# Performance work log

Hardware: AMD Instinct MI355X
Metric: run time of the kernel (lower is better)

## Reference

```python
import jax, jax.numpy as jnp
import numpy as np

B, TQ, TK, N = 4, 128, 512, 1024   # batch, query len, key len, key_size
QS, VS, OS = 1024, 1024, 1024      # query_size, value_size, output_size


def setup_inputs() -> dict:
    key = jax.random.key(0)
    ks = jax.random.split(key, 9)
    s_q = 1.0 / np.sqrt(QS)
    s_k = 1.0 / np.sqrt(N)
    s_o = 1.0 / np.sqrt(QS + VS)
    return {
        "query": jax.random.normal(ks[0], (B, TQ, QS), jnp.float32),
        "keys": jax.random.normal(ks[1], (B, TK, N), jnp.float32),
        "values": jax.random.normal(ks[2], (B, TK, VS), jnp.float32),
        # linear_q: query_size -> key_size
        "Wq": jax.random.normal(ks[3], (N, QS), jnp.float32) * s_q,
        "bq": jax.random.normal(ks[4], (N,), jnp.float32) * s_q,
        # linear_att: key_size -> 1
        "w_att": jax.random.normal(ks[5], (N,), jnp.float32) * s_k,
        "b_att": jax.random.normal(ks[6], (), jnp.float32) * s_k,
        # linear_out: (query_size + value_size) -> output_size
        "Wout": jax.random.normal(ks[7], (OS, QS + VS), jnp.float32) * s_o,
        "bout": jax.random.normal(ks[8], (OS,), jnp.float32) * s_o,
    }


def reference(query, keys, values, Wq, bq, w_att, b_att, Wout, bout):
    # linear_q: [b, t_q, query_size] -> [b, t_q, n]
    att_query = jnp.einsum("bqe,ne->bqn", query, Wq) + bq
    # Bahdanau additive score: tanh(q + k) then linear_att (n -> 1)
    # intermediate is [b, t_q, t_k, n] as in the original module
    sum_qk = jnp.tanh(att_query[:, :, None, :] + keys[:, None, :, :])
    scores = jnp.einsum("bqkn,n->bqk", sum_qk, w_att) + b_att  # [b, t_q, t_k]
    scores_normalized = jax.nn.softmax(scores, axis=2)
    # context = softmax(scores) @ values  (dropout is identity with p=0)
    context = jnp.einsum("bqk,bkv->bqv", scores_normalized, values)
    # linear_out on concat([query, context]) + tanh
    cat = jnp.concatenate([query, context], axis=2)  # [b, t_q, q+v]
    out = jnp.tanh(jnp.einsum("bqc,oc->bqo", cat, Wout) + bout)
    return out, scores_normalized
```

## Files before the change

### kernel.cpp

```cpp
#include <hip/hip_runtime.h>
#include <math.h>

static constexpr int B_  = 4;
static constexpr int TQ  = 128;
static constexpr int TK  = 512;
static constexpr int NN  = 1024;
static constexpr int QS  = 1024;
static constexpr int VS  = 1024;
static constexpr int OS  = 1024;

#define K2F    2.8853900817779268f
#define LOG2EF 1.4426950408889634f
#define SLICE  524288

typedef __attribute__((ext_vector_type(8))) short bf16x8;
typedef __attribute__((ext_vector_type(4))) float f32x4;

#define MFMA16(a,b,c) __builtin_amdgcn_mfma_f32_16x16x32_bf16((a),(b),(c),0,0,0)

__device__ __forceinline__ ushort bf16_rne(float x) {
    uint u = __float_as_uint(x);
    u += 0x7FFFu + ((u >> 16) & 1u);
    return (ushort)(u >> 16);
}
__device__ __forceinline__ void split2(float x, ushort& h, ushort& l) {
    ushort hh = bf16_rne(x);
    float hv = __uint_as_float((uint)hh << 16);
    h = hh;
    l = bf16_rne(x - hv);
}

__global__ __launch_bounds__(256) void cvt_all_kernel(
    const float* __restrict__ Q, const float* __restrict__ Wq,
    const float* __restrict__ Wo, const float* __restrict__ V,
    ushort* __restrict__ Qh, ushort* __restrict__ Ql,
    ushort* __restrict__ Wqh, ushort* __restrict__ Wql,
    ushort* __restrict__ Woh,
    ushort* __restrict__ Vth, ushort* __restrict__ Vtl)
{
    __shared__ float tile[64][65];
    const int bid = blockIdx.x;
    const int t = threadIdx.x;
    if (bid < 3584) {
        if (bid < 1536) {
            const float* src; ushort *h, *l; int idx;
            if (bid < 512) { src = Q;  h = Qh;  l = Ql;  idx = bid*256 + t; }
            else           { src = Wq; h = Wqh; l = Wql; idx = (bid-512)*256 + t; }
            float4 v = ((const float4*)src)[idx];
            ushort4 hh, ll;
            split2(v.x, hh.x, ll.x); split2(v.y, hh.y, ll.y);
            split2(v.z, hh.z, ll.z); split2(v.w, hh.w, ll.w);
            ((ushort4*)h)[idx] = hh;
            ((ushort4*)l)[idx] = ll;
        } else {
            int idx = (bid-1536)*256 + t;
            float4 v = ((const float4*)Wo)[idx];
            ushort4 hh;
            hh.x = bf16_rne(v.x); hh.y = bf16_rne(v.y);
            hh.z = bf16_rne(v.z); hh.w = bf16_rne(v.w);
            ((ushort4*)Woh)[idx] = hh;
        }
        return;
    }
    const int vid = bid - 3584;
    const int v0 = (vid & 15) * 64;
    const int k0 = ((vid >> 4) & 7) * 64;
    const int b  = vid >> 7;
    const float* src = V + ((size_t)b*TK + k0)*VS + v0;
    #pragma unroll
    for (int p = 0; p < 4; ++p) {
        int r = (t >> 4) + p*16, c = (t & 15) * 4;
        float4 vv = *(const float4*)(src + (size_t)r*VS + c);
        tile[r][c] = vv.x; tile[r][c+1] = vv.y; tile[r][c+2] = vv.z; tile[r][c+3] = vv.w;
    }
    __syncthreads();
    ushort* dh = Vth + (size_t)b*(VS*TK) + (size_t)v0*TK + k0;
    ushort* dl = Vtl + (size_t)b*(VS*TK) + (size_t)v0*TK + k0;
    #pragma unroll
    for (int p = 0; p < 4; ++p) {
        int vr = (t >> 4) + p*16, kc = (t & 15) * 4;
        ushort4 hh, ll;
        split2(tile[kc+0][vr], hh.x, ll.x);
        split2(tile[kc+1][vr], hh.y, ll.y);
        split2(tile[kc+2][vr], hh.z, ll.z);
        split2(tile[kc+3][vr], hh.w, ll.w);
        *(ushort4*)(dh + (size_t)vr*TK + kc) = hh;
        *(ushort4*)(dl + (size_t)vr*TK + kc) = ll;
    }
}

__global__ __launch_bounds__(256) void mfma_nt_kernel(
    const ushort* __restrict__ Ah, const ushort* __restrict__ Al,
    const ushort* __restrict__ Bh, const ushort* __restrict__ Bl,
    float* __restrict__ Cp, int lda, int ldb, int Nout, int kchunk, int bstride)
{
    __shared__ alignas(16) ushort lA[2][64][40];
    __shared__ alignas(16) ushort lB[2][64][40];
    const int t = threadIdx.x;
    const int m0 = blockIdx.y * 64, n0 = blockIdx.x * 64, kz = blockIdx.z;
    const int k0 = kz * kchunk;
    const int batch = m0 >> 7;
    const ushort* bhp = Bh + (size_t)batch * bstride;
    const ushort* blp = Bl + (size_t)batch * bstride;
    const int srow = t >> 2, skc = (t & 3) * 8;
    const int lane = t & 63, w = t >> 6;
    const int wm = (w >> 1) * 32, wn = (w & 1) * 32;
    const int fr = lane & 15, fg = (lane >> 4) * 8;

    f32x4 acc00 = {0,0,0,0}, acc01 = {0,0,0,0}, acc10 = {0,0,0,0}, acc11 = {0,0,0,0};

    for (int kb = k0; kb < k0 + kchunk; kb += 32) {
        uint4 va_h = *(const uint4*)(Ah  + (size_t)(m0+srow)*lda + kb + skc);
        uint4 va_l = *(const uint4*)(Al  + (size_t)(m0+srow)*lda + kb + skc);
        uint4 vb_h = *(const uint4*)(bhp + (size_t)(n0+srow)*ldb + kb + skc);
        uint4 vb_l = *(const uint4*)(blp + (size_t)(n0+srow)*ldb + kb + skc);
        *(uint4*)&lA[0][srow][skc] = va_h;
        *(uint4*)&lA[1][srow][skc] = va_l;
        *(uint4*)&lB[0][srow][skc] = vb_h;
        *(uint4*)&lB[1][srow][skc] = vb_l;
        __syncthreads();
        bf16x8 ah0 = *(const bf16x8*)&lA[0][wm + fr     ][fg];
        bf16x8 ah1 = *(const bf16x8*)&lA[0][wm + 16 + fr][fg];
        bf16x8 al0 = *(const bf16x8*)&lA[1][wm + fr     ][fg];
        bf16x8 al1 = *(const bf16x8*)&lA[1][wm + 16 + fr][fg];
        bf16x8 bh0 = *(const bf16x8*)&lB[0][wn + fr     ][fg];
        bf16x8 bh1 = *(const bf16x8*)&lB[0][wn + 16 + fr][fg];
        bf16x8 bl0 = *(const bf16x8*)&lB[1][wn + fr     ][fg];
        bf16x8 bl1 = *(const bf16x8*)&lB[1][wn + 16 + fr][fg];
        acc00 = MFMA16(ah0, bh0, acc00);
        acc00 = MFMA16(al0, bh0, acc00);
        acc00 = MFMA16(ah0, bl0, acc00);
        acc01 = MFMA16(ah0, bh1, acc01);
        acc01 = MFMA16(al0, bh1, acc01);
        acc01 = MFMA16(ah0, bl1, acc01);
        acc10 = MFMA16(ah1, bh0, acc10);
        acc10 = MFMA16(al1, bh0, acc10);
        acc10 = MFMA16(ah1, bl0, acc10);
        acc11 = MFMA16(ah1, bh1, acc11);
        acc11 = MFMA16(al1, bh1, acc11);
        acc11 = MFMA16(ah1, bl1, acc11);
        __syncthreads();
    }
    float* o = Cp + (size_t)kz * 512 * Nout;
    const int orow = (lane >> 4) * 4;
    #pragma unroll
    for (int r2 = 0; r2 < 4; ++r2) {
        o[(size_t)(m0+wm+orow+r2)*Nout      + n0+wn+fr]      = acc00[r2];
        o[(size_t)(m0+wm+orow+r2)*Nout      + n0+wn+16+fr]   = acc01[r2];
        o[(size_t)(m0+wm+16+orow+r2)*Nout   + n0+wn+fr]      = acc10[r2];
        o[(size_t)(m0+wm+16+orow+r2)*Nout   + n0+wn+16+fr]   = acc11[r2];
    }
}

__global__ __launch_bounds__(256) void exp_combine_kernel(
    const float* __restrict__ Ap, const float* __restrict__ bias,
    float* __restrict__ E)
{
    int i = blockIdx.x * 256 + threadIdx.x;
    float4 p0 = ((const float4*)Ap)[i];
    float4 p1 = ((const float4*)(Ap + SLICE))[i];
    float4 p2 = ((const float4*)(Ap + 2*SLICE))[i];
    float4 p3 = ((const float4*)(Ap + 3*SLICE))[i];
    float4 bb = ((const float4*)bias)[i & 255];
    float4 r;
    r.x = exp2f((p0.x+p1.x+p2.x+p3.x+bb.x) * K2F);
    r.y = exp2f((p0.y+p1.y+p2.y+p3.y+bb.y) * K2F);
    r.z = exp2f((p0.z+p1.z+p2.z+p3.z+bb.z) * K2F);
    r.w = exp2f((p0.w+p1.w+p2.w+p3.w+bb.w) * K2F);
    ((float4*)E)[i] = r;
}

__global__ __launch_bounds__(256) void score_v7_kernel(
    const float* __restrict__ Ea,
    const float* __restrict__ keys,
    const float* __restrict__ watt,
    float* __restrict__ Sp)
{
    __shared__ float ea[64][66];
    __shared__ float ek[64][36];
    __shared__ float wl[64];
    const int tid = threadIdx.x;
    const int kt = blockIdx.x;
    const int qt = blockIdx.y;
    const int nh = blockIdx.z;
    const int nbeg = nh * 64;
    const int q0 = qt * 64;
    const int b  = qt >> 1;
    const int k0 = b*TK + kt*32;

    {
        const int q = tid >> 2;
        const int nc = (tid & 3) * 16;
        const float* ep = Ea + (size_t)(q0 + q)*NN + nbeg + nc;
        #pragma unroll
        for (int j4 = 0; j4 < 4; ++j4) {
            float4 ev = *(const float4*)(ep + j4*4);
            ea[nc+j4*4+0][q] = ev.x;
            ea[nc+j4*4+1][q] = ev.y;
            ea[nc+j4*4+2][q] = ev.z;
            ea[nc+j4*4+3][q] = ev.w;
        }
    }
    {
        const int k = tid >> 3;
        const int nc = (tid & 7) * 8;
        const float* kp = keys + (size_t)(k0 + k)*NN + nbeg + nc;
        #pragma unroll
        for (int j4 = 0; j4 < 2; ++j4) {
            float4 kv = *(const float4*)(kp + j4*4);
            ek[nc+j4*4+0][k] = exp2f(kv.x * K2F);
            ek[nc+j4*4+1][k] = exp2f(kv.y * K2F);
            ek[nc+j4*4+2][k] = exp2f(kv.z * K2F);
            ek[nc+j4*4+3][k] = exp2f(kv.w * K2F);
        }
    }
    if (tid < 64) wl[tid] = watt[nbeg + tid];
    __syncthreads();

    const int tx = tid & 7;
    const int ty = tid >> 3;
    float acc[2][4] = {};
    #pragma unroll 4
    for (int g = 0; g < 16; ++g) {
        float2 e0 = *(const float2*)&ea[4*g+0][ty*2];
        float2 e1 = *(const float2*)&ea[4*g+1][ty*2];
        float2 e2 = *(const float2*)&ea[4*g+2][ty*2];
        float2 e3 = *(const float2*)&ea[4*g+3][ty*2];
        float4 f0 = *(const float4*)&ek[4*g+0][tx*4];
        float4 f1 = *(const float4*)&ek[4*g+1][tx*4];
        float4 f2 = *(const float4*)&ek[4*g+2][tx*4];
        float4 f3 = *(const float4*)&ek[4*g+3][tx*4];
        float4 w4 = *(const float4*)&wl[4*g];
        float E0[2] = {e0.x, e0.y};
        float E1[2] = {e1.x, e1.y};
        float E2[2] = {e2.x, e2.y};
        float E3[2] = {e3.x, e3.y};
        float F0[4] = {f0.x, f0.y, f0.z, f0.w};
        float F1[4] = {f1.x, f1.y, f1.z, f1.w};
        float F2[4] = {f2.x, f2.y, f2.z, f2.w};
        float F3[4] = {f3.x, f3.y, f3.z, f3.w};
        #pragma unroll
        for (int i = 0; i < 2; ++i) {
            #pragma unroll
            for (int j = 0; j < 4; ++j) {
                float A  = fmaf(E0[i], F0[j], 1.0f);
                float Bv = fmaf(E1[i], F1[j], 1.0f);
                float C  = fmaf(E2[i], F2[j], 1.0f);
                float D  = fmaf(E3[i], F3[j], 1.0f);
                float n0 = fmaf(w4.x, Bv, w4.y * A);
                float n1 = fmaf(w4.z, D,  w4.w * C);
                acc[i][j] = fmaf(n0, __builtin_amdgcn_rcpf(A * Bv), acc[i][j]);
                acc[i][j] = fmaf(n1, __builtin_amdgcn_rcpf(C * D),  acc[i][j]);
            }
        }
    }
    float* o = Sp + ((size_t)nh*512 + q0 + ty*2)*TK + kt*32 + tx*4;
    #pragma unroll
    for (int i = 0; i < 2; ++i) {
        float4 r = {-2.0f*acc[i][0], -2.0f*acc[i][1], -2.0f*acc[i][2], -2.0f*acc[i][3]};
        *(float4*)(o + (size_t)i*TK) = r;
    }
}

__global__ __launch_bounds__(256) void softmax_kernel(
    const float* __restrict__ Sp, float* __restrict__ P,
    ushort* __restrict__ Ph, ushort* __restrict__ Pl)
{
    const int lane = threadIdx.x & 63;
    const int wid  = threadIdx.x >> 6;
    const int row  = blockIdx.x * 4 + wid;
    const size_t S = (size_t)512*512;
    float v[8];
    float m = -3.4e38f;
    #pragma unroll
    for (int j = 0; j < 8; ++j) {
        int k = lane + j*64;
        float s = 0.f;
        #pragma unroll
        for (int h = 0; h < 16; ++h)
            s += Sp[h*S + (size_t)row*TK + k];
        v[j] = s;
        m = fmaxf(m, v[j]);
    }
    #pragma unroll
    for (int off = 32; off; off >>= 1) m = fmaxf(m, __shfl_xor(m, off, 64));
    float sum = 0.f;
    #pragma unroll
    for (int j = 0; j < 8; ++j) { v[j] = exp2f((v[j] - m) * LOG2EF); sum += v[j]; }
    #pragma unroll
    for (int off = 32; off; off >>= 1) sum += __shfl_xor(sum, off, 64);
    float inv = 1.0f / sum;
    #pragma unroll
    for (int j = 0; j < 8; ++j) {
        int k = lane + j*64;
        float pv = v[j] * inv;
        P[(size_t)row * TK + k] = pv;
        ushort h, l; split2(pv, h, l);
        Ph[(size_t)row * TK + k] = h;
        Pl[(size_t)row * TK + k] = l;
    }
}

__global__ __launch_bounds__(256) void combine_cvt_kernel(
    const float* __restrict__ Ep, ushort* __restrict__ Ch, ushort* __restrict__ Cl)
{
    int i = blockIdx.x * 256 + threadIdx.x;
    float4 p0 = ((const float4*)Ep)[i];
    float4 p1 = ((const float4*)(Ep + SLICE))[i];
    float4 p2 = ((const float4*)(Ep + 2*SLICE))[i];
    float4 p3 = ((const float4*)(Ep + 3*SLICE))[i];
    float4 s = {p0.x+p1.x+p2.x+p3.x, p0.y+p1.y+p2.y+p3.y,
                p0.z+p1.z+p2.z+p3.z, p0.w+p1.w+p2.w+p3.w};
    ushort4 hh, ll;
    split2(s.x, hh.x, ll.x); split2(s.y, hh.y, ll.y);
    split2(s.z, hh.z, ll.z); split2(s.w, hh.w, ll.w);
    ((ushort4*)Ch)[i] = hh;
    ((ushort4*)Cl)[i] = ll;
}

__global__ __launch_bounds__(256) void mfma_out_kernel(
    const ushort* __restrict__ Qh, const ushort* __restrict__ Ql,
    const ushort* __restrict__ Cxh, const ushort* __restrict__ Cxl,
    const ushort* __restrict__ Wh,
    float* __restrict__ Fp)
{
    __shared__ alignas(16) ushort lA[2][64][40];
    __shared__ alignas(16) ushort lB[64][40];
    const int t = threadIdx.x;
    const int m0 = blockIdx.y * 64, n0 = blockIdx.x * 64, kz = blockIdx.z;
    const ushort* ah_p = (kz < 2) ? Qh : Cxh;
    const ushort* al_p = (kz < 2) ? Ql : Cxl;
    const int akoff = (kz & 1) * 512;
    const int bkoff = kz * 512;
    const int srow = t >> 2, skc = (t & 3) * 8;
    const int lane = t & 63, w = t >> 6;
    const int wm = (w >> 1) * 32, wn = (w & 1) * 32;
    const int fr = lane & 15, fg = (lane >> 4) * 8;

    f32x4 acc00 = {0,0,0,0}, acc01 = {0,0,0,0}, acc10 = {0,0,0,0}, acc11 = {0,0,0,0};

    for (int kk = 0; kk < 512; kk += 32) {
        size_t aoff = (size_t)(m0+srow)*1024 + akoff + kk + skc;
        *(uint4*)&lA[0][srow][skc] = *(const uint4*)(ah_p + aoff);
        *(uint4*)&lA[1][srow][skc] = *(const uint4*)(al_p + aoff);
        *(uint4*)&lB[srow][skc] =
            *(const uint4*)(Wh + (size_t)(n0+srow)*2048 + bkoff + kk + skc);
        __syncthreads();
        bf16x8 ah0 = *(const bf16x8*)&lA[0][wm + fr     ][fg];
        bf16x8 ah1 = *(const bf16x8*)&lA[0][wm + 16 + fr][fg];
        bf16x8 al0 = *(const bf16x8*)&lA[1][wm + fr     ][fg];
        bf16x8 al1 = *(const bf16x8*)&lA[1][wm + 16 + fr][fg];
        bf16x8 bh0 = *(const bf16x8*)&lB[wn + fr     ][fg];
        bf16x8 bh1 = *(const bf16x8*)&lB[wn + 16 + fr][fg];
        acc00 = MFMA16(ah0, bh0, acc00);
        acc00 = MFMA16(al0, bh0, acc00);
        acc01 = MFMA16(ah0, bh1, acc01);
        acc01 = MFMA16(al0, bh1, acc01);
        acc10 = MFMA16(ah1, bh0, acc10);
        acc10 = MFMA16(al1, bh0, acc10);
        acc11 = MFMA16(ah1, bh1, acc11);
        acc11 = MFMA16(al1, bh1, acc11);
        __syncthreads();
    }
    float* o = Fp + (size_t)kz * SLICE;
    const int orow = (lane >> 4) * 4;
    #pragma unroll
    for (int r2 = 0; r2 < 4; ++r2) {
        o[(size_t)(m0+wm+orow+r2)*1024    + n0+wn+fr]    = acc00[r2];
        o[(size_t)(m0+wm+orow+r2)*1024    + n0+wn+16+fr] = acc01[r2];
        o[(size_t)(m0+wm+16+orow+r2)*1024 + n0+wn+fr]    = acc10[r2];
        o[(size_t)(m0+wm+16+orow+r2)*1024 + n0+wn+16+fr] = acc11[r2];
    }
}

__global__ __launch_bounds__(256) void tanh_combine_kernel(
    const float* __restrict__ Fp, const float* __restrict__ bias,
    float* __restrict__ out)
{
    int i = blockIdx.x * 256 + threadIdx.x;
    const size_t S = (size_t)B_*TQ*OS;
    float4 p0 = ((const float4*)Fp)[i];
    float4 p1 = ((const float4*)(Fp + S))[i];
    float4 p2 = ((const float4*)(Fp + 2*S))[i];
    float4 p3 = ((const float4*)(Fp + 3*S))[i];
    float4 bb = ((const float4*)bias)[i & 255];
    float4 r;
    r.x = tanhf(p0.x + p1.x + p2.x + p3.x + bb.x);
    r.y = tanhf(p0.y + p1.y + p2.y + p3.y + bb.y);
    r.z = tanhf(p0.z + p1.z + p2.z + p3.z + bb.z);
    r.w = tanhf(p0.w + p1.w + p2.w + p3.w + bb.w);
    ((float4*)out)[i] = r;
}

extern "C" void kernel_launch(void* const* d_in, const int* in_sizes, int n_in,
                              void* d_out, int out_size, void* d_ws, size_t ws_size,
                              hipStream_t stream)
{
    const float* query  = (const float*)d_in[0];
    const float* keys   = (const float*)d_in[1];
    const float* values = (const float*)d_in[2];
    const float* Wq     = (const float*)d_in[3];
    const float* bq     = (const float*)d_in[4];
    const float* watt   = (const float*)d_in[5];
    const float* Wout   = (const float*)d_in[7];
    const float* bout   = (const float*)d_in[8];

    float* out = (float*)d_out;
    float* P   = out + (size_t)B_*TQ*OS;

    char* base = (char*)d_ws;
    const size_t MB = 1u << 20;
    ushort* Qh  = (ushort*)(base +  0*MB);
    ushort* Ql  = (ushort*)(base +  1*MB);
    ushort* Wqh = (ushort*)(base +  2*MB);
    ushort* Wql = (ushort*)(base +  4*MB);
    ushort* Woh = (ushort*)(base +  6*MB);
    ushort* Vth = (ushort*)(base + 10*MB);
    ushort* Vtl = (ushort*)(base + 14*MB);
    float*  Ap  = (float*) (base + 18*MB);
    float*  Ea  = (float*) (base + 26*MB);
    float*  Sp  = (float*) (base + 28*MB);
    ushort* Ph  = (ushort*)(base + 44*MB);
    ushort* Pl  = (ushort*)(base + 44*MB + 512*1024);
    float*  Ep  = (float*) (base + 45*MB);
    ushort* Cxh = (ushort*)(base + 53*MB);
    ushort* Cxl = (ushort*)(base + 54*MB);
    float*  Fp  = (float*) (base + 55*MB);

    cvt_all_kernel<<<dim3(4096), dim3(256), 0, stream>>>(
        query, Wq, Wout, values, Qh, Ql, Wqh, Wql, Woh, Vth, Vtl);
    mfma_nt_kernel<<<dim3(16, 8, 4), dim3(256), 0, stream>>>(
        Qh, Ql, Wqh, Wql, Ap, 1024, 1024, 1024, 256, 0);
    exp_combine_kernel<<<dim3(512), dim3(256), 0, stream>>>(Ap, bq, Ea);
    score_v7_kernel<<<dim3(16, 8, 16), dim3(256), 0, stream>>>(Ea, keys, watt, Sp);
    softmax_kernel<<<dim3(128), dim3(256), 0, stream>>>(Sp, P, Ph, Pl);
    mfma_nt_kernel<<<dim3(16, 8, 4), dim3(256), 0, stream>>>(
        Ph, Pl, Vth, Vtl, Ep, 512, 512, 1024, 128, VS*TK);
    combine_cvt_kernel<<<dim3(512), dim3(256), 0, stream>>>(Ep, Cxh, Cxl);
    mfma_out_kernel<<<dim3(16, 8, 4), dim3(256), 0, stream>>>(
        Qh, Ql, Cxh, Cxl, Woh, Fp);
    tanh_combine_kernel<<<dim3(512), dim3(256), 0, stream>>>(Fp, bout, out);
}
```

Measured before the change: 82.99 us.

## Drop low bf16 half of values and halve score partial-sum slices

The values tensor is now converted only to a high bf16 part. The P·V GEMM uses a new kernel that does two MFMAs per tile pair (Ph·Vh, Pl·Vh) instead of three, and the Vtl buffer and its writes are removed. Separately, each score block now covers two 64-wide n chunks in sequence, so there are 8 partial slices instead of 16, which reduces Sp traffic and the number of reads the softmax must sum. This trades some accuracy in the context product and some score-kernel parallelism for less memory traffic and less MFMA work.

```diff
diff --git a/kernel.cpp b/kernel.cpp
--- a/kernel.cpp
+++ b/kernel.cpp
@@ -36,7 +36,7 @@
     ushort* __restrict__ Qh, ushort* __restrict__ Ql,
     ushort* __restrict__ Wqh, ushort* __restrict__ Wql,
     ushort* __restrict__ Woh,
-    ushort* __restrict__ Vth, ushort* __restrict__ Vtl)
+    ushort* __restrict__ Vth)
 {
     __shared__ float tile[64][65];
     const int bid = blockIdx.x;
@@ -75,17 +75,15 @@
     }
     __syncthreads();
     ushort* dh = Vth + (size_t)b*(VS*TK) + (size_t)v0*TK + k0;
-    ushort* dl = Vtl + (size_t)b*(VS*TK) + (size_t)v0*TK + k0;
     #pragma unroll
     for (int p = 0; p < 4; ++p) {
         int vr = (t >> 4) + p*16, kc = (t & 15) * 4;
-        ushort4 hh, ll;
-        split2(tile[kc+0][vr], hh.x, ll.x);
-        split2(tile[kc+1][vr], hh.y, ll.y);
-        split2(tile[kc+2][vr], hh.z, ll.z);
-        split2(tile[kc+3][vr], hh.w, ll.w);
+        ushort4 hh;
+        hh.x = bf16_rne(tile[kc+0][vr]);
+        hh.y = bf16_rne(tile[kc+1][vr]);
+        hh.z = bf16_rne(tile[kc+2][vr]);
+        hh.w = bf16_rne(tile[kc+3][vr]);
         *(ushort4*)(dh + (size_t)vr*TK + kc) = hh;
-        *(ushort4*)(dl + (size_t)vr*TK + kc) = ll;
     }
 }
 
@@ -152,186 +150,18 @@
     }
 }
 
-__global__ __launch_bounds__(256) void exp_combine_kernel(
-    const float* __restrict__ Ap, const float* __restrict__ bias,
-    float* __restrict__ E)
-{
-    int i = blockIdx.x * 256 + threadIdx.x;
-    float4 p0 = ((const float4*)Ap)[i];
-    float4 p1 = ((const float4*)(Ap + SLICE))[i];
-    float4 p2 = ((const float4*)(Ap + 2*SLICE))[i];
-    float4 p3 = ((const float4*)(Ap + 3*SLICE))[i];
-    float4 bb = ((const float4*)bias)[i & 255];
-    float4 r;
-    r.x = exp2f((p0.x+p1.x+p2.x+p3.x+bb.x) * K2F);
-    r.y = exp2f((p0.y+p1.y+p2.y+p3.y+bb.y) * K2F);
-    r.z = exp2f((p0.z+p1.z+p2.z+p3.z+bb.z) * K2F);
-    r.w = exp2f((p0.w+p1.w+p2.w+p3.w+bb.w) * K2F);
-    ((float4*)E)[i] = r;
-}
-
-__global__ __launch_bounds__(256) void score_v7_kernel(
-    const float* __restrict__ Ea,
-    const float* __restrict__ keys,
-    const float* __restrict__ watt,
-    float* __restrict__ Sp)
-{
-    __shared__ float ea[64][66];
-    __shared__ float ek[64][36];
-    __shared__ float wl[64];
-    const int tid = threadIdx.x;
-    const int kt = blockIdx.x;
-    const int qt = blockIdx.y;
-    const int nh = blockIdx.z;
-    const int nbeg = nh * 64;
-    const int q0 = qt * 64;
-    const int b  = qt >> 1;
-    const int k0 = b*TK + kt*32;
-
-    {
-        const int q = tid >> 2;
-        const int nc = (tid & 3) * 16;
-        const float* ep = Ea + (size_t)(q0 + q)*NN + nbeg + nc;
-        #pragma unroll
-        for (int j4 = 0; j4 < 4; ++j4) {
-            float4 ev = *(const float4*)(ep + j4*4);
-            ea[nc+j4*4+0][q] = ev.x;
-            ea[nc+j4*4+1][q] = ev.y;
-            ea[nc+j4*4+2][q] = ev.z;
-            ea[nc+j4*4+3][q] = ev.w;
-        }
-    }
-    {
-        const int k = tid >> 3;
-        const int nc = (tid & 7) * 8;
-        const float* kp = keys + (size_t)(k0 + k)*NN + nbeg + nc;
-        #pragma unroll
-        for (int j4 = 0; j4 < 2; ++j4) {
-            float4 kv = *(const float4*)(kp + j4*4);
-            ek[nc+j4*4+0][k] = exp2f(kv.x * K2F);
-            ek[nc+j4*4+1][k] = exp2f(kv.y * K2F);
-            ek[nc+j4*4+2][k] = exp2f(kv.z * K2F);
-            ek[nc+j4*4+3][k] = exp2f(kv.w * K2F);
-        }
-    }
-    if (tid < 64) wl[tid] = watt[nbeg + tid];
-    __syncthreads();
-
-    const int tx = tid & 7;
-    const int ty = tid >> 3;
-    float acc[2][4] = {};
-    #pragma unroll 4
-    for (int g = 0; g < 16; ++g) {
-        float2 e0 = *(const float2*)&ea[4*g+0][ty*2];
-        float2 e1 = *(const float2*)&ea[4*g+1][ty*2];
-        float2 e2 = *(const float2*)&ea[4*g+2][ty*2];
-        float2 e3 = *(const float2*)&ea[4*g+3][ty*2];
-        float4 f0 = *(const float4*)&ek[4*g+0][tx*4];
-        float4 f1 = *(const float4*)&ek[4*g+1][tx*4];
-        float4 f2 = *(const float4*)&ek[4*g+2][tx*4];
-        float4 f3 = *(const float4*)&ek[4*g+3][tx*4];
-        float4 w4 = *(const float4*)&wl[4*g];
-        float E0[2] = {e0.x, e0.y};
-        float E1[2] = {e1.x, e1.y};
-        float E2[2] = {e2.x, e2.y};
-        float E3[2] = {e3.x, e3.y};
-        float F0[4] = {f0.x, f0.y, f0.z, f0.w};
-        float F1[4] = {f1.x, f1.y, f1.z, f1.w};
-        float F2[4] = {f2.x, f2.y, f2.z, f2.w};
-        float F3[4] = {f3.x, f3.y, f3.z, f3.w};
-        #pragma unroll
-        for (int i = 0; i < 2; ++i) {
-            #pragma unroll
-            for (int j = 0; j < 4; ++j) {
-                float A  = fmaf(E0[i], F0[j], 1.0f);
-                float Bv = fmaf(E1[i], F1[j], 1.0f);
-                float C  = fmaf(E2[i], F2[j], 1.0f);
-                float D  = fmaf(E3[i], F3[j], 1.0f);
-                float n0 = fmaf(w4.x, Bv, w4.y * A);
-                float n1 = fmaf(w4.z, D,  w4.w * C);
-                acc[i][j] = fmaf(n0, __builtin_amdgcn_rcpf(A * Bv), acc[i][j]);
-                acc[i][j] = fmaf(n1, __builtin_amdgcn_rcpf(C * D),  acc[i][j]);
-            }
-        }
-    }
-    float* o = Sp + ((size_t)nh*512 + q0 + ty*2)*TK + kt*32 + tx*4;
-    #pragma unroll
-    for (int i = 0; i < 2; ++i) {
-        float4 r = {-2.0f*acc[i][0], -2.0f*acc[i][1], -2.0f*acc[i][2], -2.0f*acc[i][3]};
-        *(float4*)(o + (size_t)i*TK) = r;
-    }
-}
-
-__global__ __launch_bounds__(256) void softmax_kernel(
-    const float* __restrict__ Sp, float* __restrict__ P,
-    ushort* __restrict__ Ph, ushort* __restrict__ Pl)
-{
-    const int lane = threadIdx.x & 63;
-    const int wid  = threadIdx.x >> 6;
-    const int row  = blockIdx.x * 4 + wid;
-    const size_t S = (size_t)512*512;
-    float v[8];
-    float m = -3.4e38f;
-    #pragma unroll
-    for (int j = 0; j < 8; ++j) {
-        int k = lane + j*64;
-        float s = 0.f;
-        #pragma unroll
-        for (int h = 0; h < 16; ++h)
-            s += Sp[h*S + (size_t)row*TK + k];
-        v[j] = s;
-        m = fmaxf(m, v[j]);
-    }
-    #pragma unroll
-    for (int off = 32; off; off >>= 1) m = fmaxf(m, __shfl_xor(m, off, 64));
-    float sum = 0.f;
-    #pragma unroll
-    for (int j = 0; j < 8; ++j) { v[j] = exp2f((v[j] - m) * LOG2EF); sum += v[j]; }
-    #pragma unroll
-    for (int off = 32; off; off >>= 1) sum += __shfl_xor(sum, off, 64);
-    float inv = 1.0f / sum;
-    #pragma unroll
-    for (int j = 0; j < 8; ++j) {
-        int k = lane + j*64;
-        float pv = v[j] * inv;
-        P[(size_t)row * TK + k] = pv;
-        ushort h, l; split2(pv, h, l);
-        Ph[(size_t)row * TK + k] = h;
-        Pl[(size_t)row * TK + k] = l;
-    }
-}
-
-__global__ __launch_bounds__(256) void combine_cvt_kernel(
-    const float* __restrict__ Ep, ushort* __restrict__ Ch, ushort* __restrict__ Cl)
-{
-    int i = blockIdx.x * 256 + threadIdx.x;
-    float4 p0 = ((const float4*)Ep)[i];
-    float4 p1 = ((const float4*)(Ep + SLICE))[i];
-    float4 p2 = ((const float4*)(Ep + 2*SLICE))[i];
-    float4 p3 = ((const float4*)(Ep + 3*SLICE))[i];
-    float4 s = {p0.x+p1.x+p2.x+p3.x, p0.y+p1.y+p2.y+p3.y,
-                p0.z+p1.z+p2.z+p3.z, p0.w+p1.w+p2.w+p3.w};
-    ushort4 hh, ll;
-    split2(s.x, hh.x, ll.x); split2(s.y, hh.y, ll.y);
-    split2(s.z, hh.z, ll.z); split2(s.w, hh.w, ll.w);
-    ((ushort4*)Ch)[i] = hh;
-    ((ushort4*)Cl)[i] = ll;
-}
-
-__global__ __launch_bounds__(256) void mfma_out_kernel(
-    const ushort* __restrict__ Qh, const ushort* __restrict__ Ql,
-    const ushort* __restrict__ Cxh, const ushort* __restrict__ Cxl,
-    const ushort* __restrict__ Wh,
-    float* __restrict__ Fp)
+__global__ __launch_bounds__(256) void mfma_nt2_kernel(
+    const ushort* __restrict__ Ah, const ushort* __restrict__ Al,
+    const ushort* __restrict__ Bh,
+    float* __restrict__ Cp, int lda, int ldb, int Nout, int kchunk, int bstride)
 {
     __shared__ alignas(16) ushort lA[2][64][40];
     __shared__ alignas(16) ushort lB[64][40];
     const int t = threadIdx.x;
     const int m0 = blockIdx.y * 64, n0 = blockIdx.x * 64, kz = blockIdx.z;
-    const ushort* ah_p = (kz < 2) ? Qh : Cxh;
-    const ushort* al_p = (kz < 2) ? Ql : Cxl;
-    const int akoff = (kz & 1) * 512;
-    const int bkoff = kz * 512;
+    const int k0 = kz * kchunk;
+    const int batch = m0 >> 7;
+    const ushort* bhp = Bh + (size_t)batch * bstride;
     const int srow = t >> 2, skc = (t & 3) * 8;
     const int lane = t & 63, w = t >> 6;
     const int wm = (w >> 1) * 32, wn = (w & 1) * 32;
@@ -339,12 +169,10 @@
 
     f32x4 acc00 = {0,0,0,0}, acc01 = {0,0,0,0}, acc10 = {0,0,0,0}, acc11 = {0,0,0,0};
 
-    for (int kk = 0; kk < 512; kk += 32) {
-        size_t aoff = (size_t)(m0+srow)*1024 + akoff + kk + skc;
-        *(uint4*)&lA[0][srow][skc] = *(const uint4*)(ah_p + aoff);
-        *(uint4*)&lA[1][srow][skc] = *(const uint4*)(al_p + aoff);
-        *(uint4*)&lB[srow][skc] =
-            *(const uint4*)(Wh + (size_t)(n0+srow)*2048 + bkoff + kk + skc);
+    for (int kb = k0; kb < k0 + kchunk; kb += 32) {
+        *(uint4*)&lA[0][srow][skc] = *(const uint4*)(Ah  + (size_t)(m0+srow)*lda + kb + skc);
+        *(uint4*)&lA[1][srow][skc] = *(const uint4*)(Al  + (size_t)(m0+srow)*lda + kb + skc);
+        *(uint4*)&lB[srow][skc]    = *(const uint4*)(bhp + (size_t)(n0+srow)*ldb + kb + skc);
         __syncthreads();
         bf16x8 ah0 = *(const bf16x8*)&lA[0][wm + fr     ][fg];
         bf16x8 ah1 = *(const bf16x8*)&lA[0][wm + 16 + fr][fg];
@@ -362,6 +190,231 @@
         acc11 = MFMA16(al1, bh1, acc11);
         __syncthreads();
     }
+    float* o = Cp + (size_t)kz * 512 * Nout;
+    const int orow = (lane >> 4) * 4;
+    #pragma unroll
+    for (int r2 = 0; r2 < 4; ++r2) {
+        o[(size_t)(m0+wm+orow+r2)*Nout      + n0+wn+fr]      = acc00[r2];
+        o[(size_t)(m0+wm+orow+r2)*Nout      + n0+wn+16+fr]   = acc01[r2];
+        o[(size_t)(m0+wm+16+orow+r2)*Nout   + n0+wn+fr]      = acc10[r2];
+        o[(size_t)(m0+wm+16+orow+r2)*Nout   + n0+wn+16+fr]   = acc11[r2];
+    }
+}
+
+__global__ __launch_bounds__(256) void exp_combine_kernel(
+    const float* __restrict__ Ap, const float* __restrict__ bias,
+    float* __restrict__ E)
+{
+    int i = blockIdx.x * 256 + threadIdx.x;
+    float4 p0 = ((const float4*)Ap)[i];
+    float4 p1 = ((const float4*)(Ap + SLICE))[i];
+    float4 p2 = ((const float4*)(Ap + 2*SLICE))[i];
+    float4 p3 = ((const float4*)(Ap + 3*SLICE))[i];
+    float4 bb = ((const float4*)bias)[i & 255];
+    float4 r;
+    r.x = exp2f((p0.x+p1.x+p2.x+p3.x+bb.x) * K2F);
+    r.y = exp2f((p0.y+p1.y+p2.y+p3.y+bb.y) * K2F);
+    r.z = exp2f((p0.z+p1.z+p2.z+p3.z+bb.z) * K2F);
+    r.w = exp2f((p0.w+p1.w+p2.w+p3.w+bb.w) * K2F);
+    ((float4*)E)[i] = r;
+}
+
+__global__ __launch_bounds__(256) void score_v8_kernel(
+    const float* __restrict__ Ea,
+    const float* __restrict__ keys,
+    const float* __restrict__ watt,
+    float* __restrict__ Sp)
+{
+    __shared__ float ea[64][66];
+    __shared__ float ek[64][36];
+    __shared__ float wl[64];
+    const int tid = threadIdx.x;
+    const int kt = blockIdx.x;
+    const int qt = blockIdx.y;
+    const int nh = blockIdx.z;
+    const int q0 = qt * 64;
+    const int b  = qt >> 1;
+    const int k0 = b*TK + kt*32;
+    const int tx = tid & 7;
+    const int ty = tid >> 3;
+    float acc[2][4] = {};
+
+    #pragma unroll
+    for (int half = 0; half < 2; ++half) {
+        const int nbeg = nh*128 + half*64;
+        if (half) __syncthreads();
+        {
+            const int q = tid >> 2;
+            const int nc = (tid & 3) * 16;
+            const float* ep = Ea + (size_t)(q0 + q)*NN + nbeg + nc;
+            #pragma unroll
+            for (int j4 = 0; j4 < 4; ++j4) {
+                float4 ev = *(const float4*)(ep + j4*4);
+                ea[nc+j4*4+0][q] = ev.x;
+                ea[nc+j4*4+1][q] = ev.y;
+                ea[nc+j4*4+2][q] = ev.z;
+                ea[nc+j4*4+3][q] = ev.w;
+            }
+        }
+        {
+            const int k = tid >> 3;
+            const int nc = (tid & 7) * 8;
+            const float* kp = keys + (size_t)(k0 + k)*NN + nbeg + nc;
+            #pragma unroll
+            for (int j4 = 0; j4 < 2; ++j4) {
+                float4 kv = *(const float4*)(kp + j4*4);
+                ek[nc+j4*4+0][k] = exp2f(kv.x * K2F);
+                ek[nc+j4*4+1][k] = exp2f(kv.y * K2F);
+                ek[nc+j4*4+2][k] = exp2f(kv.z * K2F);
+                ek[nc+j4*4+3][k] = exp2f(kv.w * K2F);
+            }
+        }
+        if (tid < 64) wl[tid] = watt[nbeg + tid];
+        __syncthreads();
+
+        #pragma unroll 4
+        for (int g = 0; g < 16; ++g) {
+            float2 e0 = *(const float2*)&ea[4*g+0][ty*2];
+            float2 e1 = *(const float2*)&ea[4*g+1][ty*2];
+            float2 e2 = *(const float2*)&ea[4*g+2][ty*2];
+            float2 e3 = *(const float2*)&ea[4*g+3][ty*2];
+            float4 f0 = *(const float4*)&ek[4*g+0][tx*4];
+            float4 f1 = *(const float4*)&ek[4*g+1][tx*4];
+            float4 f2 = *(const float4*)&ek[4*g+2][tx*4];
+            float4 f3 = *(const float4*)&ek[4*g+3][tx*4];
+            float4 w4 = *(const float4*)&wl[4*g];
+            float E0[2] = {e0.x, e0.y};
+            float E1[2] = {e1.x, e1.y};
+            float E2[2] = {e2.x, e2.y};
+            float E3[2] = {e3.x, e3.y};
+            float F0[4] = {f0.x, f0.y, f0.z, f0.w};
+            float F1[4] = {f1.x, f1.y, f1.z, f1.w};
+            float F2[4] = {f2.x, f2.y, f2.z, f2.w};
+            float F3[4] = {f3.x, f3.y, f3.z, f3.w};
+            #pragma unroll
+            for (int i = 0; i < 2; ++i) {
+                #pragma unroll
+                for (int j = 0; j < 4; ++j) {
+                    float A  = fmaf(E0[i], F0[j], 1.0f);
+                    float Bv = fmaf(E1[i], F1[j], 1.0f);
+                    float C  = fmaf(E2[i], F2[j], 1.0f);
+                    float D  = fmaf(E3[i], F3[j], 1.0f);
+                    float n0 = fmaf(w4.x, Bv, w4.y * A);
+                    float n1 = fmaf(w4.z, D,  w4.w * C);
+                    acc[i][j] = fmaf(n0, __builtin_amdgcn_rcpf(A * Bv), acc[i][j]);
+                    acc[i][j] = fmaf(n1, __builtin_amdgcn_rcpf(C * D),  acc[i][j]);
+                }
+            }
+        }
+    }
+    float* o = Sp + ((size_t)nh*512 + q0 + ty*2)*TK + kt*32 + tx*4;
+    #pragma unroll
+    for (int i = 0; i < 2; ++i) {
+        float4 r = {-2.0f*acc[i][0], -2.0f*acc[i][1], -2.0f*acc[i][2], -2.0f*acc[i][3]};
+        *(float4*)(o + (size_t)i*TK) = r;
+    }
+}
+
+__global__ __launch_bounds__(256) void softmax_kernel(
+    const float* __restrict__ Sp, float* __restrict__ P,
+    ushort* __restrict__ Ph, ushort* __restrict__ Pl)
+{
+    const int lane = threadIdx.x & 63;
+    const int wid  = threadIdx.x >> 6;
+    const int row  = blockIdx.x * 4 + wid;
+    const size_t S = (size_t)512*512;
+    float v[8];
+    float m = -3.4e38f;
+    #pragma unroll
+    for (int j = 0; j < 8; ++j) {
+        int k = lane + j*64;
+        float s = 0.f;
+        #pragma unroll
+        for (int h = 0; h < 8; ++h)
+            s += Sp[h*S + (size_t)row*TK + k];
+        v[j] = s;
+        m = fmaxf(m, v[j]);
+    }
+    #pragma unroll
+    for (int off = 32; off; off >>= 1) m = fmaxf(m, __shfl_xor(m, off, 64));
+    float sum = 0.f;
+    #pragma unroll
+    for (int j = 0; j < 8; ++j) { v[j] = exp2f((v[j] - m) * LOG2EF); sum += v[j]; }
+    #pragma unroll
+    for (int off = 32; off; off >>= 1) sum += __shfl_xor(sum, off, 64);
+    float inv = 1.0f / sum;
+    #pragma unroll
+    for (int j = 0; j < 8; ++j) {
+        int k = lane + j*64;
+        float pv = v[j] * inv;
+        P[(size_t)row * TK + k] = pv;
+        ushort h, l; split2(pv, h, l);
+        Ph[(size_t)row * TK + k] = h;
+        Pl[(size_t)row * TK + k] = l;
+    }
+}
+
+__global__ __launch_bounds__(256) void combine_cvt_kernel(
+    const float* __restrict__ Ep, ushort* __restrict__ Ch, ushort* __restrict__ Cl)
+{
+    int i = blockIdx.x * 256 + threadIdx.x;
+    float4 p0 = ((const float4*)Ep)[i];
+    float4 p1 = ((const float4*)(Ep + SLICE))[i];
+    float4 p2 = ((const float4*)(Ep + 2*SLICE))[i];
+    float4 p3 = ((const float4*)(Ep + 3*SLICE))[i];
+    float4 s = {p0.x+p1.x+p2.x+p3.x, p0.y+p1.y+p2.y+p3.y,
+                p0.z+p1.z+p2.z+p3.z, p0.w+p1.w+p2.w+p3.w};
+    ushort4 hh, ll;
+    split2(s.x, hh.x, ll.x); split2(s.y, hh.y, ll.y);
+    split2(s.z, hh.z, ll.z); split2(s.w, hh.w, ll.w);
+    ((ushort4*)Ch)[i] = hh;
+    ((ushort4*)Cl)[i] = ll;
+}
+
+__global__ __launch_bounds__(256) void mfma_out_kernel(
+    const ushort* __restrict__ Qh, const ushort* __restrict__ Ql,
+    const ushort* __restrict__ Cxh, const ushort* __restrict__ Cxl,
+    const ushort* __restrict__ Wh,
+    float* __restrict__ Fp)
+{
+    __shared__ alignas(16) ushort lA[2][64][40];
+    __shared__ alignas(16) ushort lB[64][40];
+    const int t = threadIdx.x;
+    const int m0 = blockIdx.y * 64, n0 = blockIdx.x * 64, kz = blockIdx.z;
+    const ushort* ah_p = (kz < 2) ? Qh : Cxh;
+    const ushort* al_p = (kz < 2) ? Ql : Cxl;
+    const int akoff = (kz & 1) * 512;
+    const int bkoff = kz * 512;
+    const int srow = t >> 2, skc = (t & 3) * 8;
+    const int lane = t & 63, w = t >> 6;
+    const int wm = (w >> 1) * 32, wn = (w & 1) * 32;
+    const int fr = lane & 15, fg = (lane >> 4) * 8;
+
+    f32x4 acc00 = {0,0,0,0}, acc01 = {0,0,0,0}, acc10 = {0,0,0,0}, acc11 = {0,0,0,0};
+
+    for (int kk = 0; kk < 512; kk += 32) {
+        size_t aoff = (size_t)(m0+srow)*1024 + akoff + kk + skc;
+        *(uint4*)&lA[0][srow][skc] = *(const uint4*)(ah_p + aoff);
+        *(uint4*)&lA[1][srow][skc] = *(const uint4*)(al_p + aoff);
+        *(uint4*)&lB[srow][skc] =
+            *(const uint4*)(Wh + (size_t)(n0+srow)*2048 + bkoff + kk + skc);
+        __syncthreads();
+        bf16x8 ah0 = *(const bf16x8*)&lA[0][wm + fr     ][fg];
+        bf16x8 ah1 = *(const bf16x8*)&lA[0][wm + 16 + fr][fg];
+        bf16x8 al0 = *(const bf16x8*)&lA[1][wm + fr     ][fg];
+        bf16x8 al1 = *(const bf16x8*)&lA[1][wm + 16 + fr][fg];
+        bf16x8 bh0 = *(const bf16x8*)&lB[wn + fr     ][fg];
+        bf16x8 bh1 = *(const bf16x8*)&lB[wn + 16 + fr][fg];
+        acc00 = MFMA16(ah0, bh0, acc00);
+        acc00 = MFMA16(al0, bh0, acc00);
+        acc01 = MFMA16(ah0, bh1, acc01);
+        acc01 = MFMA16(al0, bh1, acc01);
+        acc10 = MFMA16(ah1, bh0, acc10);
+        acc10 = MFMA16(al1, bh0, acc10);
+        acc11 = MFMA16(ah1, bh1, acc11);
+        acc11 = MFMA16(al1, bh1, acc11);
+        __syncthreads();
+    }
     float* o = Fp + (size_t)kz * SLICE;
     const int orow = (lane >> 4) * 4;
     #pragma unroll
@@ -416,26 +469,25 @@
     ushort* Wql = (ushort*)(base +  4*MB);
     ushort* Woh = (ushort*)(base +  6*MB);
     ushort* Vth = (ushort*)(base + 10*MB);
-    ushort* Vtl = (ushort*)(base + 14*MB);
-    float*  Ap  = (float*) (base + 18*MB);
-    float*  Ea  = (float*) (base + 26*MB);
-    float*  Sp  = (float*) (base + 28*MB);
-    ushort* Ph  = (ushort*)(base + 44*MB);
-    ushort* Pl  = (ushort*)(base + 44*MB + 512*1024);
-    float*  Ep  = (float*) (base + 45*MB);
-    ushort* Cxh = (ushort*)(base + 53*MB);
-    ushort* Cxl = (ushort*)(base + 54*MB);
-    float*  Fp  = (float*) (base + 55*MB);
+    float*  Ap  = (float*) (base + 14*MB);
+    float*  Ea  = (float*) (base + 22*MB);
+    float*  Sp  = (float*) (base + 24*MB);
+    ushort* Ph  = (ushort*)(base + 32*MB);
+    ushort* Pl  = (ushort*)(base + 32*MB + 512*1024);
+    float*  Ep  = (float*) (base + 33*MB);
+    ushort* Cxh = (ushort*)(base + 41*MB);
+    ushort* Cxl = (ushort*)(base + 42*MB);
+    float*  Fp  = (float*) (base + 43*MB);
 
     cvt_all_kernel<<<dim3(4096), dim3(256), 0, stream>>>(
-        query, Wq, Wout, values, Qh, Ql, Wqh, Wql, Woh, Vth, Vtl);
+        query, Wq, Wout, values, Qh, Ql, Wqh, Wql, Woh, Vth);
     mfma_nt_kernel<<<dim3(16, 8, 4), dim3(256), 0, stream>>>(
         Qh, Ql, Wqh, Wql, Ap, 1024, 1024, 1024, 256, 0);
     exp_combine_kernel<<<dim3(512), dim3(256), 0, stream>>>(Ap, bq, Ea);
-    score_v7_kernel<<<dim3(16, 8, 16), dim3(256), 0, stream>>>(Ea, keys, watt, Sp);
+    score_v8_kernel<<<dim3(16, 8, 8), dim3(256), 0, stream>>>(Ea, keys, watt, Sp);
     softmax_kernel<<<dim3(128), dim3(256), 0, stream>>>(Sp, P, Ph, Pl);
-    mfma_nt_kernel<<<dim3(16, 8, 4), dim3(256), 0, stream>>>(
-        Ph, Pl, Vth, Vtl, Ep, 512, 512, 1024, 128, VS*TK);
+    mfma_nt2_kernel<<<dim3(16, 8, 4), dim3(256), 0, stream>>>(
+        Ph, Pl, Vth, Ep, 512, 512, 1024, 128, VS*TK);
     combine_cvt_kernel<<<dim3(512), dim3(256), 0, stream>>>(Ep, Cxh, Cxl);
     mfma_out_kernel<<<dim3(16, 8, 4), dim3(256), 0, stream>>>(
         Qh, Ql, Cxh, Cxl, Woh, Fp);
```

Measured after the change: 81.64 us. No clear change (-1.6%).
